# Kernel tuning notes

Measured on AMD Instinct MI355X. Metric: run time of the kernel, lower is better.

Reference implementation:

```python
import jax, jax.numpy as jnp
import numpy as np
import math

DK = 768  # latent_size used for the scale (not the per-head dim, matching the original)

def setup_inputs() -> dict:
    key = jax.random.key(0)
    k1, k2, k3 = jax.random.split(key, 3)
    B, H, S, D = 4, 12, 2048, 64
    queries = jax.random.normal(k1, (B, H, S, D), dtype=jnp.float32)
    keys = jax.random.normal(k2, (B, H, S, D), dtype=jnp.float32)
    values = jax.random.normal(k3, (B, S, H, D), dtype=jnp.float32)  # note [B,S,H,D] layout
    return {"queries": queries, "keys": keys, "values": values}

def reference(queries, keys, values):
    # scores: [B,H,S,S]
    scores = jnp.einsum('bhqd,bhkd->bhqk', queries, keys) / math.sqrt(DK)
    probs = jax.nn.softmax(scores, axis=3)
    v = jnp.transpose(values, (0, 2, 1, 3))  # [B,S,H,D] -> [B,H,S,D]
    return jnp.einsum('bhqk,bhkd->bhqd', probs, v)
```

## Files before the change

kernel.cpp:

```cpp
#include <hip/hip_runtime.h>

#define SQ 2048
#define DH 64
#define NH 12
#define NBH 48
#define QTILE 128
#define KTILE 64
#define NITER (SQ / KTILE)
#define NQT (SQ / QTILE)

typedef short short8 __attribute__((ext_vector_type(8)));
typedef float f32x4  __attribute__((ext_vector_type(4)));
typedef float f32x16 __attribute__((ext_vector_type(16)));
typedef int   i32x4 __attribute__((ext_vector_type(4)));
typedef int   i32x2 __attribute__((ext_vector_type(2)));

#define MFMA32(a, b, c) __builtin_amdgcn_mfma_f32_32x32x16_bf16(a, b, c, 0, 0, 0)

typedef __attribute__((address_space(1))) const void* gas_ptr;
typedef __attribute__((address_space(3))) void* las_ptr;

__device__ __forceinline__ void load_lds16(const void* g, void* l) {
    __builtin_amdgcn_global_load_lds((gas_ptr)g, (las_ptr)l, 16, 0, 0);
}

__device__ __forceinline__ short f2bf(float f) {
    union { float f; unsigned u; } v;
    v.f = f;
    unsigned r = v.u + 0x7FFFu + ((v.u >> 16) & 1u);
    return (short)(r >> 16);
}

#if defined(__has_builtin) && __has_builtin(__builtin_amdgcn_cvt_pk_bf16_f32)
typedef __bf16 bf16x2_t __attribute__((ext_vector_type(2)));
__device__ __forceinline__ unsigned pk2bf(float a, float b) {
    bf16x2_t v = __builtin_amdgcn_cvt_pk_bf16_f32(a, b);
    union { bf16x2_t v; unsigned u; } c; c.v = v; return c.u;
}
#else
__device__ __forceinline__ unsigned pk2bf(float a, float b) {
    union { float f; unsigned u; } x, y; x.f = a; y.f = b;
    unsigned ra = x.u + 0x7FFFu + ((x.u >> 16) & 1u);
    unsigned rb = y.u + 0x7FFFu + ((y.u >> 16) & 1u);
    return (ra >> 16) | (rb & 0xFFFF0000u);
}
#endif

__global__ __launch_bounds__(256)
void convert_k(const float* __restrict__ K, short* __restrict__ Kb) {
    const size_t i = (size_t)(blockIdx.x * 256 + threadIdx.x) * 8;
    f32x4 a = *(const f32x4*)&K[i];
    f32x4 b = *(const f32x4*)&K[i + 4];
    unsigned o[4] = { pk2bf(a[0], a[1]), pk2bf(a[2], a[3]),
                      pk2bf(b[0], b[1]), pk2bf(b[2], b[3]) };
    *(i32x4*)&Kb[i] = *(i32x4*)o;
}

__global__ __launch_bounds__(256)
void transpose_v(const float* __restrict__ V, short* __restrict__ Vt) {
    __shared__ float Ls[64][68];
    const int bx = blockIdx.x;
    const int st = bx & 31;
    const int bh = bx >> 5;
    const int b = bh / NH, h = bh % NH;
    const int s0 = st * 64;
    const float* src = V + ((size_t)b * SQ * NH + (size_t)h) * DH;
    const int dg = threadIdx.x & 15;
    const int sl = threadIdx.x >> 4;
    #pragma unroll
    for (int p = 0; p < 4; ++p) {
        const int row = p * 16 + sl;
        *(f32x4*)&Ls[row][dg * 4] =
            *(const f32x4*)&src[(size_t)(s0 + row) * (NH * DH) + dg * 4];
    }
    __syncthreads();
    const int dr = threadIdx.x >> 2;
    const int sc = (threadIdx.x & 3) * 16;
    unsigned out[8];
    #pragma unroll
    for (int jj = 0; jj < 8; ++jj)
        out[jj] = pk2bf(Ls[sc + 2 * jj][dr], Ls[sc + 2 * jj + 1][dr]);
    short* dst = Vt + (size_t)bh * DH * SQ + (size_t)dr * SQ + s0 + sc;
    *(i32x4*)(dst)     = *(i32x4*)&out[0];
    *(i32x4*)(dst + 8) = *(i32x4*)&out[4];
}

__global__ __launch_bounds__(256)
void attn_fused_kernel(const float* __restrict__ Q,
                       const short* __restrict__ Kb,
                       const short* __restrict__ Vtg,
                       float* __restrict__ O) {
    __shared__ short Ks[KTILE * DH];
    __shared__ short Vs[DH * KTILE];
    __shared__ short Ps[QTILE][72];

    const int tid  = threadIdx.x;
    const int lane = tid & 63;
    const int w    = tid >> 6;
    const int m31  = lane & 31;
    const int hl   = lane >> 5;
    const int l7   = lane & 7;

    const int bx = blockIdx.x;
    const int qt = bx & (NQT - 1);
    const int bh = bx >> 4;
    const int q0 = qt * QTILE;

    const float* Qb  = Q   + (size_t)bh * SQ * DH;
    const short* Kbh = Kb  + (size_t)bh * SQ * DH;
    const short* Vbh = Vtg + (size_t)bh * DH * SQ;
    float*       Ob  = O   + (size_t)bh * SQ * DH;

    const float qscale = 0.03608439182435161f * 1.4426950408889634f;

    short8 qf[4];
    {
        const int qrow = q0 + 32 * w + m31;
        #pragma unroll
        for (int s = 0; s < 4; ++s) {
            const float* src = Qb + (size_t)qrow * DH + 16 * s + 8 * hl;
            short8 f;
            #pragma unroll
            for (int j = 0; j < 8; ++j) f[j] = f2bf(src[j] * qscale);
            qf[s] = f;
        }
    }

    const int gk = (lane & 7) ^ (lane >> 3);
    const int rr = w * 8 + (lane >> 3);
    const short* kg0 = Kbh + (size_t)rr * DH + gk * 8;
    const short* kg1 = kg0 + 32 * DH;
    const short* vg0 = Vbh + (size_t)rr * SQ + gk * 8;
    const short* vg1 = vg0 + 32 * SQ;
    char* ksb = (char*)Ks;
    char* vsb = (char*)Vs;

    int koff[4];
    #pragma unroll
    for (int s = 0; s < 4; ++s) koff[s] = (((2 * s + hl) ^ l7) * 8);
    const short* kbase = Ks + m31 * DH;
    const short* vbase = Vs + m31 * DH;
    short* prow = &Ps[32 * w + m31][0];

    f32x16 o0 = {}, o1 = {};
    float lp = 0.f;

    for (int it = 0; it < NITER; ++it) {
        const size_t ko = (size_t)it * (KTILE * DH);
        const size_t vo = (size_t)it * KTILE;
        load_lds16(kg0 + ko, ksb + w * 1024);
        load_lds16(kg1 + ko, ksb + 4096 + w * 1024);
        load_lds16(vg0 + vo, vsb + w * 1024);
        load_lds16(vg1 + vo, vsb + 4096 + w * 1024);
        __syncthreads();

        f32x16 s0 = {}, s1 = {};
        #pragma unroll
        for (int s = 0; s < 4; ++s) {
            short8 ka0 = *(const short8*)(kbase + koff[s]);
            short8 ka1 = *(const short8*)(kbase + 2048 + koff[s]);
            s0 = MFMA32(ka0, qf[s], s0);
            s1 = MFMA32(ka1, qf[s], s1);
        }

        #pragma unroll
        for (int g = 0; g < 4; ++g) {
            float p0 = __builtin_amdgcn_exp2f(s0[4 * g + 0]);
            float p1 = __builtin_amdgcn_exp2f(s0[4 * g + 1]);
            float p2 = __builtin_amdgcn_exp2f(s0[4 * g + 2]);
            float p3 = __builtin_amdgcn_exp2f(s0[4 * g + 3]);
            lp += (p0 + p1) + (p2 + p3);
            i32x2 w2 = { (int)pk2bf(p0, p1), (int)pk2bf(p2, p3) };
            *(i32x2*)(prow + 8 * g + 4 * hl) = w2;
        }
        #pragma unroll
        for (int g = 0; g < 4; ++g) {
            float p0 = __builtin_amdgcn_exp2f(s1[4 * g + 0]);
            float p1 = __builtin_amdgcn_exp2f(s1[4 * g + 1]);
            float p2 = __builtin_amdgcn_exp2f(s1[4 * g + 2]);
            float p3 = __builtin_amdgcn_exp2f(s1[4 * g + 3]);
            lp += (p0 + p1) + (p2 + p3);
            i32x2 w2 = { (int)pk2bf(p0, p1), (int)pk2bf(p2, p3) };
            *(i32x2*)(prow + 32 + 8 * g + 4 * hl) = w2;
        }

        #pragma unroll
        for (int s = 0; s < 4; ++s) {
            short8 pa  = *(const short8*)(prow + 16 * s + 8 * hl);
            short8 vb0 = *(const short8*)(vbase + koff[s]);
            short8 vb1 = *(const short8*)(vbase + 2048 + koff[s]);
            o0 = MFMA32(pa, vb0, o0);
            o1 = MFMA32(pa, vb1, o1);
        }
        __syncthreads();
    }

    float v = lp;
    v += __shfl_xor(v, 32, 64);
    const float linv = 1.0f / v;

    #pragma unroll
    for (int dt = 0; dt < 2; ++dt) {
        const f32x16& o = dt ? o1 : o0;
        #pragma unroll
        for (int reg = 0; reg < 16; ++reg) {
            const int qp = (reg & 3) + 8 * (reg >> 2) + 4 * hl;
            const float rl = __shfl(linv, qp, 64);
            const int q = q0 + 32 * w + qp;
            Ob[(size_t)q * DH + 32 * dt + m31] = o[reg] * rl;
        }
    }
}

extern "C" void kernel_launch(void* const* d_in, const int* in_sizes, int n_in,
                              void* d_out, int out_size, void* d_ws, size_t ws_size,
                              hipStream_t stream) {
    const float* Q = (const float*)d_in[0];
    const float* K = (const float*)d_in[1];
    const float* V = (const float*)d_in[2];
    float* O = (float*)d_out;

    short* Kb  = (short*)d_ws;
    short* Vtg = Kb + (size_t)NBH * SQ * DH;

    convert_k<<<dim3(NBH * SQ * DH / 8 / 256), dim3(256), 0, stream>>>(K, Kb);
    transpose_v<<<dim3(NBH * 32), dim3(256), 0, stream>>>(V, Vtg);
    attn_fused_kernel<<<dim3(NBH * NQT), dim3(256), 0, stream>>>(Q, Kb, Vtg, O);
}
```

Baseline: 185.1 us.

## Double-buffer K/V tiles, keep P in registers, merge prepass kernels

Merges the K-convert and V-transpose kernels into one launch. K/V tiles are now double-buffered in LDS, so the next tile's load is issued while the current one is computed, and the trailing barrier is dropped. The P tile now goes from the S accumulator to the PV MFMA A-operand through cross-half lane shuffles instead of an LDS round-trip. Launch bounds ask for 3 blocks per CU. The changes remove a kernel launch, LDS traffic and one barrier per iteration, at the cost of more LDS per block and extra shuffle instructions. A single barrier per iteration must protect buffer reuse, and that needs checking.

```diff
diff --git a/kernel.cpp b/kernel.cpp
--- a/kernel.cpp
+++ b/kernel.cpp
@@ -13,7 +13,6 @@
 typedef float f32x4  __attribute__((ext_vector_type(4)));
 typedef float f32x16 __attribute__((ext_vector_type(16)));
 typedef int   i32x4 __attribute__((ext_vector_type(4)));
-typedef int   i32x2 __attribute__((ext_vector_type(2)));
 
 #define MFMA32(a, b, c) __builtin_amdgcn_mfma_f32_32x32x16_bf16(a, b, c, 0, 0, 0)
 
@@ -46,20 +45,21 @@
 }
 #endif
 
+#define KCONV_BLOCKS (NBH * SQ * DH / 8 / 256)
 __global__ __launch_bounds__(256)
-void convert_k(const float* __restrict__ K, short* __restrict__ Kb) {
-    const size_t i = (size_t)(blockIdx.x * 256 + threadIdx.x) * 8;
-    f32x4 a = *(const f32x4*)&K[i];
-    f32x4 b = *(const f32x4*)&K[i + 4];
-    unsigned o[4] = { pk2bf(a[0], a[1]), pk2bf(a[2], a[3]),
-                      pk2bf(b[0], b[1]), pk2bf(b[2], b[3]) };
-    *(i32x4*)&Kb[i] = *(i32x4*)o;
-}
-
-__global__ __launch_bounds__(256)
-void transpose_v(const float* __restrict__ V, short* __restrict__ Vt) {
+void prepass(const float* __restrict__ K, short* __restrict__ Kb,
+             const float* __restrict__ V, short* __restrict__ Vt) {
     __shared__ float Ls[64][68];
-    const int bx = blockIdx.x;
+    if (blockIdx.x < KCONV_BLOCKS) {
+        const size_t i = (size_t)(blockIdx.x * 256 + threadIdx.x) * 8;
+        f32x4 a = *(const f32x4*)&K[i];
+        f32x4 b = *(const f32x4*)&K[i + 4];
+        unsigned o[4] = { pk2bf(a[0], a[1]), pk2bf(a[2], a[3]),
+                          pk2bf(b[0], b[1]), pk2bf(b[2], b[3]) };
+        *(i32x4*)&Kb[i] = *(i32x4*)o;
+        return;
+    }
+    const int bx = blockIdx.x - KCONV_BLOCKS;
     const int st = bx & 31;
     const int bh = bx >> 5;
     const int b = bh / NH, h = bh % NH;
@@ -85,14 +85,13 @@
     *(i32x4*)(dst + 8) = *(i32x4*)&out[4];
 }
 
-__global__ __launch_bounds__(256)
+__global__ __launch_bounds__(256, 3)
 void attn_fused_kernel(const float* __restrict__ Q,
                        const short* __restrict__ Kb,
                        const short* __restrict__ Vtg,
                        float* __restrict__ O) {
-    __shared__ short Ks[KTILE * DH];
-    __shared__ short Vs[DH * KTILE];
-    __shared__ short Ps[QTILE][72];
+    __shared__ short Ks[2][KTILE * DH];
+    __shared__ short Vs[2][DH * KTILE];
 
     const int tid  = threadIdx.x;
     const int lane = tid & 63;
@@ -132,27 +131,33 @@
     const short* kg1 = kg0 + 32 * DH;
     const short* vg0 = Vbh + (size_t)rr * SQ + gk * 8;
     const short* vg1 = vg0 + 32 * SQ;
-    char* ksb = (char*)Ks;
-    char* vsb = (char*)Vs;
 
     int koff[4];
     #pragma unroll
     for (int s = 0; s < 4; ++s) koff[s] = (((2 * s + hl) ^ l7) * 8);
-    const short* kbase = Ks + m31 * DH;
-    const short* vbase = Vs + m31 * DH;
-    short* prow = &Ps[32 * w + m31][0];
 
     f32x16 o0 = {}, o1 = {};
     float lp = 0.f;
 
+    #define ISSUE(itx, buf) do {                                           \
+        const size_t ko_ = (size_t)(itx) * (KTILE * DH);                   \
+        const size_t vo_ = (size_t)(itx) * KTILE;                          \
+        char* kb_ = (char*)Ks[buf]; char* vb_ = (char*)Vs[buf];            \
+        load_lds16(kg0 + ko_, kb_ + w * 1024);                             \
+        load_lds16(kg1 + ko_, kb_ + 4096 + w * 1024);                      \
+        load_lds16(vg0 + vo_, vb_ + w * 1024);                             \
+        load_lds16(vg1 + vo_, vb_ + 4096 + w * 1024);                      \
+    } while (0)
+
+    ISSUE(0, 0);
+
     for (int it = 0; it < NITER; ++it) {
-        const size_t ko = (size_t)it * (KTILE * DH);
-        const size_t vo = (size_t)it * KTILE;
-        load_lds16(kg0 + ko, ksb + w * 1024);
-        load_lds16(kg1 + ko, ksb + 4096 + w * 1024);
-        load_lds16(vg0 + vo, vsb + w * 1024);
-        load_lds16(vg1 + vo, vsb + 4096 + w * 1024);
         __syncthreads();
+        const int cur = it & 1;
+        if (it + 1 < NITER) ISSUE(it + 1, cur ^ 1);
+
+        const short* kbase = Ks[cur] + m31 * DH;
+        const short* vbase = Vs[cur] + m31 * DH;
 
         f32x16 s0 = {}, s1 = {};
         #pragma unroll
@@ -163,37 +168,40 @@
             s1 = MFMA32(ka1, qf[s], s1);
         }
 
-        #pragma unroll
-        for (int g = 0; g < 4; ++g) {
-            float p0 = __builtin_amdgcn_exp2f(s0[4 * g + 0]);
-            float p1 = __builtin_amdgcn_exp2f(s0[4 * g + 1]);
-            float p2 = __builtin_amdgcn_exp2f(s0[4 * g + 2]);
-            float p3 = __builtin_amdgcn_exp2f(s0[4 * g + 3]);
-            lp += (p0 + p1) + (p2 + p3);
-            i32x2 w2 = { (int)pk2bf(p0, p1), (int)pk2bf(p2, p3) };
-            *(i32x2*)(prow + 8 * g + 4 * hl) = w2;
-        }
-        #pragma unroll
-        for (int g = 0; g < 4; ++g) {
-            float p0 = __builtin_amdgcn_exp2f(s1[4 * g + 0]);
-            float p1 = __builtin_amdgcn_exp2f(s1[4 * g + 1]);
-            float p2 = __builtin_amdgcn_exp2f(s1[4 * g + 2]);
-            float p3 = __builtin_amdgcn_exp2f(s1[4 * g + 3]);
-            lp += (p0 + p1) + (p2 + p3);
-            i32x2 w2 = { (int)pk2bf(p0, p1), (int)pk2bf(p2, p3) };
-            *(i32x2*)(prow + 32 + 8 * g + 4 * hl) = w2;
+        short8 pfrag[4];
+        #pragma unroll
+        for (int half = 0; half < 2; ++half) {
+            const f32x16& sv = half ? s1 : s0;
+            #pragma unroll
+            for (int wd = 0; wd < 2; ++wd) {
+                float p[8];
+                #pragma unroll
+                for (int j = 0; j < 8; ++j)
+                    p[j] = __builtin_amdgcn_exp2f(sv[8 * wd + j]);
+                lp += ((p[0] + p[1]) + (p[2] + p[3])) +
+                      ((p[4] + p[5]) + (p[6] + p[7]));
+                unsigned a0 = pk2bf(p[0], p[1]);
+                unsigned a1 = pk2bf(p[2], p[3]);
+                unsigned b0 = pk2bf(p[4], p[5]);
+                unsigned b1 = pk2bf(p[6], p[7]);
+                unsigned r0 = (unsigned)__shfl_xor((int)(hl ? a0 : b0), 32, 64);
+                unsigned r1 = (unsigned)__shfl_xor((int)(hl ? a1 : b1), 32, 64);
+                union { unsigned u[4]; short8 v; } fr;
+                if (hl == 0) { fr.u[0] = a0; fr.u[1] = a1; fr.u[2] = r0; fr.u[3] = r1; }
+                else         { fr.u[0] = r0; fr.u[1] = r1; fr.u[2] = b0; fr.u[3] = b1; }
+                pfrag[2 * half + wd] = fr.v;
+            }
         }
 
         #pragma unroll
         for (int s = 0; s < 4; ++s) {
-            short8 pa  = *(const short8*)(prow + 16 * s + 8 * hl);
             short8 vb0 = *(const short8*)(vbase + koff[s]);
             short8 vb1 = *(const short8*)(vbase + 2048 + koff[s]);
-            o0 = MFMA32(pa, vb0, o0);
-            o1 = MFMA32(pa, vb1, o1);
-        }
-        __syncthreads();
-    }
+            o0 = MFMA32(pfrag[s], vb0, o0);
+            o1 = MFMA32(pfrag[s], vb1, o1);
+        }
+    }
+    #undef ISSUE
 
     float v = lp;
     v += __shfl_xor(v, 32, 64);
@@ -223,7 +231,6 @@
     short* Kb  = (short*)d_ws;
     short* Vtg = Kb + (size_t)NBH * SQ * DH;
 
-    convert_k<<<dim3(NBH * SQ * DH / 8 / 256), dim3(256), 0, stream>>>(K, Kb);
-    transpose_v<<<dim3(NBH * 32), dim3(256), 0, stream>>>(V, Vtg);
+    prepass<<<dim3(KCONV_BLOCKS + NBH * 32), dim3(256), 0, stream>>>(K, Kb, V, Vtg);
     attn_fused_kernel<<<dim3(NBH * NQT), dim3(256), 0, stream>>>(Q, Kb, Vtg, O);
 }
```

Result: faster. 180.6 us (-2.4%).
